# Kernel tuning notes

Measured on AMD Instinct MI355X. Metric: run time of the kernel, lower is better.

## Reference

```python
import jax, jax.numpy as jnp
import numpy as np

ALPHA = 0.2   # LeakyReLU negative slope
BN_EPS = 1e-5
NEG_INF = -9e15  # same masking constant as the torch source


def make_quaternion_mul(kernel):
    # kernel: [in_features//4, out_features]; returns hamilton [in_features, out_features]
    r, i, j, k = jnp.split(kernel, 4, axis=1)
    r2 = jnp.concatenate([r, -i, -j, -k], axis=1)
    i2 = jnp.concatenate([i,  r, -k,  j], axis=1)
    j2 = jnp.concatenate([j,  k,  r, -i], axis=1)
    k2 = jnp.concatenate([k, -j,  i,  r], axis=1)
    return jnp.concatenate([r2, i2, j2, k2], axis=0)


def setup_inputs() -> dict:
    key = jax.random.key(0)
    k1, k2, k3, k4 = jax.random.split(key, 4)
    N, IN_F, OUT_F = 8192, 1024, 256
    inp = jax.random.normal(k1, (N, IN_F), dtype=jnp.float32)
    adj = jax.random.randint(k2, (N, N), 0, 2, dtype=jnp.int32)
    # xavier-uniform-like init scales
    W = jax.random.uniform(k3, (IN_F // 4, OUT_F), dtype=jnp.float32,
                           minval=-1.0, maxval=1.0) * np.sqrt(6.0 / (IN_F // 4 + OUT_F))
    a = jax.random.uniform(k4, (2 * OUT_F, 1), dtype=jnp.float32,
                           minval=-1.0, maxval=1.0) * np.sqrt(6.0 / (2 * OUT_F + 1))
    gamma = jnp.ones((OUT_F,), dtype=jnp.float32)
    beta = jnp.zeros((OUT_F,), dtype=jnp.float32)
    return {"input": inp, "adj": adj, "W": W, "a": a, "gamma": gamma, "beta": beta}


def reference(input, adj, W, a, gamma, beta):
    hamilton = make_quaternion_mul(W)            # [IN_F, OUT_F]
    h = input @ hamilton                         # [N, OUT_F]
    F_out = h.shape[1]
    # e[i, j] = leakyrelu(concat(h_i, h_j) . a) = leakyrelu(h_i.a1 + h_j.a2)
    a1 = a[:F_out, 0]
    a2 = a[F_out:, 0]
    e = jax.nn.leaky_relu((h @ a1)[:, None] + (h @ a2)[None, :],
                          negative_slope=ALPHA)  # [N, N]
    e = jnp.where(adj > 0, e, NEG_INF)
    attention = jax.nn.softmax(e, axis=1)        # masked softmax over neighbors
    h_prime = attention @ h                      # [N, OUT_F]
    # BatchNorm1d (training mode: batch statistics, biased variance)
    mean = jnp.mean(h_prime, axis=0)
    var = jnp.var(h_prime, axis=0)
    h_norm = (h_prime - mean) * jax.lax.rsqrt(var + BN_EPS) * gamma + beta
    return jax.nn.elu(h_norm)                    # concat=True -> elu
```

## Files before the change

### kernel.cpp

```cpp
#include <hip/hip_runtime.h>
#include <stdint.h>

#define ALPHA 0.2f
#define LOG2E 1.4426950408889634f

typedef __attribute__((ext_vector_type(8))) short short8;
typedef __attribute__((ext_vector_type(4))) float f32x4;
typedef __attribute__((ext_vector_type(16))) float f32x16;
typedef __attribute__((ext_vector_type(4))) int int4v;
typedef __attribute__((ext_vector_type(2))) unsigned int uint2v;

#if __has_builtin(__builtin_amdgcn_exp2f)
#define EXP2(x) __builtin_amdgcn_exp2f(x)
#else
#define EXP2(x) exp2f(x)
#endif

__device__ __forceinline__ unsigned short f2bf(float x){
  union { float f; uint32_t u; } v; v.f = x;
  uint32_t u = v.u;
  u += 0x7FFFu + ((u >> 16) & 1u);
  return (unsigned short)(u >> 16);
}
__device__ __forceinline__ float bf2f(unsigned short s){
  union { uint32_t u; float f; } v; v.u = ((uint32_t)s) << 16; return v.f;
}
__device__ __forceinline__ unsigned encf(float x){
  unsigned u = __float_as_uint(x);
  return (u & 0x80000000u) ? ~u : (u | 0x80000000u);
}
__device__ __forceinline__ float decf(unsigned u){
  return (u & 0x80000000u) ? __uint_as_float(u & 0x7FFFFFFFu) : __uint_as_float(~u);
}

__global__ void k_ham(const float* __restrict__ W, unsigned short* __restrict__ hi,
                      unsigned short* __restrict__ lo, unsigned* __restrict__ S2enc,
                      float* __restrict__ gsum, float* __restrict__ gsumsq){
  if (blockIdx.x == 0){
    if (threadIdx.x == 0) S2enc[0] = 0u;
    gsum[threadIdx.x] = 0.f; gsumsq[threadIdx.x] = 0.f;
  }
  int id = blockIdx.x * 256 + threadIdx.x;
  int c = id >> 10, k = id & 1023;
  int b = k >> 8, r = k & 255;
  int cb = c >> 6, col = c & 63;
  const int   comp[4][4] = {{0,1,2,3},{1,0,3,2},{2,3,0,1},{3,2,1,0}};
  const float sgn [4][4] = {{1.f,-1.f,-1.f,-1.f},{1.f,1.f,-1.f,1.f},
                            {1.f,1.f,1.f,-1.f},{1.f,-1.f,1.f,1.f}};
  float v = sgn[b][cb] * W[r * 256 + comp[b][cb] * 64 + col];
  unsigned short h = f2bf(v);
  hi[id] = h;
  lo[id] = f2bf(v - bf2f(h));
}

__global__ __launch_bounds__(256) void k_gemm1(
    const float* __restrict__ inp, const unsigned short* __restrict__ hamHi,
    const unsigned short* __restrict__ hamLo, const float* __restrict__ avec,
    unsigned short* __restrict__ hT, float* __restrict__ s1s, float* __restrict__ s2s,
    unsigned* __restrict__ S2enc){
  int i0 = blockIdx.x * 32;
  int w = threadIdx.x >> 6, lane = threadIdx.x & 63;
  int mi = lane & 15, g = lane >> 4;
  int cbase = w * 64;
  f32x4 acc[2][4];
#pragma unroll
  for (int mf=0; mf<2; ++mf)
#pragma unroll
    for (int nf=0; nf<4; ++nf) acc[mf][nf] = (f32x4){0.f,0.f,0.f,0.f};

  for (int k0 = 0; k0 < 1024; k0 += 32){
    short8 ah[2], al[2];
#pragma unroll
    for (int mf=0; mf<2; ++mf){
      const float* ap = inp + (size_t)(i0 + 16*mf + mi) * 1024 + k0 + 8*g;
      f32x4 x0 = *(const f32x4*)ap;
      f32x4 x1 = *(const f32x4*)(ap + 4);
#pragma unroll
      for (int e=0; e<8; ++e){
        float x = (e < 4) ? x0[e] : x1[e-4];
        unsigned short h = f2bf(x);
        ah[mf][e] = (short)h;
        al[mf][e] = (short)f2bf(x - bf2f(h));
      }
    }
    short8 bh[4], bl[4];
#pragma unroll
    for (int nf=0; nf<4; ++nf){
      size_t off = (size_t)(cbase + 16*nf + mi) * 1024 + k0 + 8*g;
      bh[nf] = *(const short8*)(hamHi + off);
      bl[nf] = *(const short8*)(hamLo + off);
    }
#pragma unroll
    for (int mf=0; mf<2; ++mf)
#pragma unroll
      for (int nf=0; nf<4; ++nf){
        acc[mf][nf] = __builtin_amdgcn_mfma_f32_16x16x32_bf16(ah[mf], bh[nf], acc[mf][nf], 0,0,0);
        acc[mf][nf] = __builtin_amdgcn_mfma_f32_16x16x32_bf16(ah[mf], bl[nf], acc[mf][nf], 0,0,0);
        acc[mf][nf] = __builtin_amdgcn_mfma_f32_16x16x32_bf16(al[mf], bh[nf], acc[mf][nf], 0,0,0);
      }
  }
  float p1[2][4] = {{0,0,0,0},{0,0,0,0}}, p2[2][4] = {{0,0,0,0},{0,0,0,0}};
#pragma unroll
  for (int nf=0; nf<4; ++nf){
    int c = cbase + 16*nf + mi;
    float a1c = avec[c], a2c = avec[256 + c];
    int Sc = (c & 7) << 3;
#pragma unroll
    for (int mf=0; mf<2; ++mf){
      int ibase = i0 + 16*mf + 4*g;
      uint2v u;
      u[0] = (uint32_t)f2bf(acc[mf][nf][0]) | ((uint32_t)f2bf(acc[mf][nf][1]) << 16);
      u[1] = (uint32_t)f2bf(acc[mf][nf][2]) | ((uint32_t)f2bf(acc[mf][nf][3]) << 16);
      *(uint2v*)(hT + (size_t)c * 8192 + (size_t)(ibase ^ Sc)) = u;
#pragma unroll
      for (int rg=0; rg<4; ++rg){
        p1[mf][rg] += acc[mf][nf][rg] * a1c;
        p2[mf][rg] += acc[mf][nf][rg] * a2c;
      }
    }
  }
#pragma unroll
  for (int off=1; off<16; off<<=1){
#pragma unroll
    for (int mf=0; mf<2; ++mf)
#pragma unroll
      for (int rg=0; rg<4; ++rg){
        p1[mf][rg] += __shfl_xor(p1[mf][rg], off);
        p2[mf][rg] += __shfl_xor(p2[mf][rg], off);
      }
  }
  __shared__ float red1[4][32], red2[4][32];
  if (mi == 0){
#pragma unroll
    for (int mf=0; mf<2; ++mf)
#pragma unroll
      for (int rg=0; rg<4; ++rg){
        red1[w][16*mf + 4*g + rg] = p1[mf][rg];
        red2[w][16*mf + 4*g + rg] = p2[mf][rg];
      }
  }
  __syncthreads();
  if (threadIdx.x < 32){
    int r = threadIdx.x;
    float v1 = red1[0][r] + red1[1][r] + red1[2][r] + red1[3][r];
    float v2 = red2[0][r] + red2[1][r] + red2[2][r] + red2[3][r];
    s1s[i0 + r] = v1 * LOG2E;
    float v2s = v2 * LOG2E;
    s2s[i0 + r] = v2s;
    float m = v2s;
#pragma unroll
    for (int off=1; off<32; off<<=1) m = fmaxf(m, __shfl_xor(m, off));
    if (r == 0) atomicMax(S2enc, encf(m));
  }
}

#define STAGE(t, b) do { \
    _Pragma("unroll") \
    for (int r_ = 0; r_ < 8; ++r_){ \
      int ch_ = tid + r_*256; \
      const unsigned short* gp_ = hT + (size_t)(ch_ >> 3)*8192 + jw0 + (t)*64 + (ch_&7)*8; \
      __builtin_amdgcn_global_load_lds((const __attribute__((address_space(1))) void*)(const void*)gp_, \
          (__attribute__((address_space(3))) void*)(void*)&hbuf[(b)][ch_*8], 16, 0, 0); \
    } } while(0)

#define ALOAD(dst, t) do { \
    _Pragma("unroll") \
    for (int ks_ = 0; ks_ < 4; ++ks_){ \
      dst[2*ks_]   = *(const int4v*)(arow + (t)*64 + ks_*16); \
      dst[2*ks_+1] = *(const int4v*)(arow + (t)*64 + ks_*16 + 4); \
    } } while(0)

__global__ __launch_bounds__(256,1) void k_attn(
    const int* __restrict__ adj, const unsigned short* __restrict__ hT,
    const float* __restrict__ s1s, const float* __restrict__ s2s,
    const unsigned* __restrict__ S2enc, float* __restrict__ accp, float* __restrict__ Zp){
  __shared__ unsigned short hbuf[2][256*64];
  __shared__ float s2l[2048];
  const int tid = threadIdx.x;
  const int id = blockIdx.x;
  const int js = (id & 7) >> 1;
  const int rb = ((id >> 3) << 1) | (id & 1);
  const int w = tid >> 6, lane = tid & 63;
  const int r31 = lane & 31, hi = lane >> 5;
  const int i0w = rb * 128 + w * 32;
  const int jw0 = js * 2048;

  { f32x4 v0 = *(const f32x4*)(s2s + jw0 + tid*8);
    f32x4 v1 = *(const f32x4*)(s2s + jw0 + tid*8 + 4);
    *(f32x4*)&s2l[tid*8] = v0; *(f32x4*)&s2l[tid*8 + 4] = v1; }

  const float S2MAX = decf(S2enc[0]);
  const float s1v = s1s[i0w + r31];
  const float xm = s1v + S2MAX;
  const float m2 = fmaxf(xm, ALPHA * xm);
  const float P1 = s1v - m2;
  const float P2 = ALPHA * s1v - m2;

  const int* arow = adj + (size_t)(i0w + r31) * 8192 + jw0 + hi*8;

  f32x16 acc[8];
#pragma unroll
  for (int nf=0; nf<8; ++nf)
#pragma unroll
    for (int q=0; q<16; ++q) acc[nf][q] = 0.f;
  float zac = 0.f;

  int4v cur[8], nxt[8];
  ALOAD(cur, 0);
  STAGE(0, 0);
  __syncthreads();

  for (int tile = 0; tile < 32; ++tile){
    const int buf = tile & 1;
    if (tile < 31){
      STAGE(tile + 1, buf ^ 1);
      ALOAD(nxt, tile + 1);
    }
#pragma unroll
    for (int ks=0; ks<4; ++ks){
      f32x4 sa = *(const f32x4*)&s2l[tile*64 + ks*16 + hi*8];
      f32x4 sb = *(const f32x4*)&s2l[tile*64 + ks*16 + hi*8 + 4];
      short8 pa;
#pragma unroll
      for (int e=0; e<8; ++e){
        float s2e = (e < 4) ? sa[e] : sb[e-4];
        float t1 = P1 + s2e;
        float t2 = fmaf(ALPHA, s2e, P2);
        float pe = EXP2(fmaxf(t1, t2));
        int ae = (e < 4) ? cur[2*ks][e] : cur[2*ks+1][e-4];
        pe = (ae > 0) ? pe : 0.f;
        zac += pe;
        pa[e] = (short)f2bf(pe);
      }
      const int xk = ks*16 + hi*8;
#pragma unroll
      for (int nf=0; nf<8; ++nf){
        const int c = 32*nf + r31;
        short8 b = *(const short8*)&hbuf[buf][c*64 + (xk ^ ((c&7)<<3))];
        acc[nf] = __builtin_amdgcn_mfma_f32_32x32x16_bf16(pa, b, acc[nf], 0,0,0);
      }
    }
    if (tile < 31){
#pragma unroll
      for (int q=0; q<8; ++q) cur[q] = nxt[q];
    }
    __syncthreads();
  }
  zac += __shfl_xor(zac, 32);
  if (lane < 32) Zp[js*8192 + i0w + lane] = zac;
#pragma unroll
  for (int nf=0; nf<8; ++nf){
    const int c = 32*nf + r31;
#pragma unroll
    for (int reg=0; reg<16; ++reg){
      const int roff = (reg&3) + 8*(reg>>2) + 4*hi;
      accp[(size_t)(js*8192 + i0w + roff)*256 + c] = acc[nf][reg];
    }
  }
}

__global__ void k_stats(const float* __restrict__ accp, const float* __restrict__ Zp,
                        float* __restrict__ hp, float* __restrict__ gsum,
                        float* __restrict__ gsumsq){
  int c = threadIdx.x;
  int r0 = blockIdx.x * 32;
  float s = 0.f, sq = 0.f;
  for (int r=0; r<32; ++r){
    int i = r0 + r;
    float z = Zp[i] + Zp[8192 + i] + Zp[16384 + i] + Zp[24576 + i];
    float inv = (z > 0.f) ? 1.f / z : 0.f;
    size_t o = (size_t)i * 256 + c;
    float v = (accp[o] + accp[o + 8192*256] + accp[o + 2*8192*256] + accp[o + 3*8192*256]) * inv;
    hp[o] = v;
    s += v; sq += v*v;
  }
  atomicAdd(&gsum[c], s);
  atomicAdd(&gsumsq[c], sq);
}

__global__ void k_bnelu(float* __restrict__ out, const float* __restrict__ gsum,
                        const float* __restrict__ gsumsq, const float* __restrict__ gamma,
                        const float* __restrict__ beta){
  int id = blockIdx.x * 256 + threadIdx.x;
  int c = id & 255;
  float mean = gsum[c] * (1.f/8192.f);
  float var  = gsumsq[c] * (1.f/8192.f) - mean*mean;
  float x = (out[id] - mean) * rsqrtf(var + 1e-5f) * gamma[c] + beta[c];
  out[id] = x > 0.f ? x : (EXP2(x * LOG2E) - 1.f);
}

extern "C" void kernel_launch(void* const* d_in, const int* in_sizes, int n_in,
                              void* d_out, int out_size, void* d_ws, size_t ws_size,
                              hipStream_t stream){
  const float* inp   = (const float*)d_in[0];
  const int*   adj   = (const int*)d_in[1];
  const float* W     = (const float*)d_in[2];
  const float* avec  = (const float*)d_in[3];
  const float* gamma = (const float*)d_in[4];
  const float* beta  = (const float*)d_in[5];
  float* out = (float*)d_out;

  char* ws = (char*)d_ws;
  float* accp = (float*)ws;
  float* Zp   = accp + 4*8192*256;
  unsigned short* hamHi = (unsigned short*)(Zp + 32768);
  unsigned short* hamLo = hamHi + 262144;
  unsigned short* hT    = hamLo + 262144;
  float* s1s = (float*)(hT + 2097152);
  float* s2s = s1s + 8192;
  unsigned* S2enc = (unsigned*)(s2s + 8192);
  float* gsum   = (float*)(S2enc + 64);
  float* gsumsq = gsum + 256;

  k_ham<<<1024, 256, 0, stream>>>(W, hamHi, hamLo, S2enc, gsum, gsumsq);
  k_gemm1<<<256, 256, 0, stream>>>(inp, hamHi, hamLo, avec, hT, s1s, s2s, S2enc);
  k_attn<<<256, 256, 0, stream>>>(adj, hT, s1s, s2s, S2enc, accp, Zp);
  k_stats<<<256, 256, 0, stream>>>(accp, Zp, out, gsum, gsumsq);
  k_bnelu<<<8192, 256, 0, stream>>>(out, gsum, gsumsq, gamma, beta);
}
```

Baseline: 192.9 us.

## Pre-pack adjacency into bitmasks in a high-occupancy pass before attention

Extra blocks are added to the first GEMM launch that convert the int32 adjacency matrix into 64-bit ballot bitmasks. The attention kernel then reads one bit per edge instead of a full int, which removes the large adj stream from the low-occupancy MFMA loop. The full adjacency read still happens once, but at high occupancy, and it costs an extra bitmask buffer plus a kernel-ordering dependency.

```diff
diff --git a/kernel.cpp b/kernel.cpp
--- a/kernel.cpp
+++ b/kernel.cpp
@@ -53,11 +53,31 @@
   lo[id] = f2bf(v - bf2f(h));
 }
 
-__global__ __launch_bounds__(256) void k_gemm1(
-    const float* __restrict__ inp, const unsigned short* __restrict__ hamHi,
-    const unsigned short* __restrict__ hamLo, const float* __restrict__ avec,
-    unsigned short* __restrict__ hT, float* __restrict__ s1s, float* __restrict__ s2s,
-    unsigned* __restrict__ S2enc){
+__global__ __launch_bounds__(256) void k_work(
+    const float* __restrict__ inp, const int* __restrict__ adj,
+    const unsigned short* __restrict__ hamHi, const unsigned short* __restrict__ hamLo,
+    const float* __restrict__ avec, unsigned short* __restrict__ hT,
+    float* __restrict__ s1s, float* __restrict__ s2s, unsigned* __restrict__ S2enc,
+    unsigned long long* __restrict__ bm){
+  if (blockIdx.x >= 256){
+    const int lane = threadIdx.x & 63;
+    const size_t wid = ((size_t)(blockIdx.x - 256) * 256 + threadIdx.x) >> 6;
+    const size_t W0 = wid * 1024;
+    unsigned long long b[16];
+#pragma unroll
+    for (int q = 0; q < 4; ++q){
+      int4v a = *(const int4v*)(adj + W0 + 256*q + 4*lane);
+#pragma unroll
+      for (int k = 0; k < 4; ++k) b[4*q + k] = __ballot(a[k] > 0);
+    }
+    if (lane < 16){
+      unsigned long long v = b[0];
+#pragma unroll
+      for (int m = 1; m < 16; ++m) v = (lane == m) ? b[m] : v;
+      bm[W0/64 + lane] = v;
+    }
+    return;
+  }
   int i0 = blockIdx.x * 32;
   int w = threadIdx.x >> 6, lane = threadIdx.x & 63;
   int mi = lane & 15, g = lane >> 4;
@@ -163,15 +183,8 @@
           (__attribute__((address_space(3))) void*)(void*)&hbuf[(b)][ch_*8], 16, 0, 0); \
     } } while(0)
 
-#define ALOAD(dst, t) do { \
-    _Pragma("unroll") \
-    for (int ks_ = 0; ks_ < 4; ++ks_){ \
-      dst[2*ks_]   = *(const int4v*)(arow + (t)*64 + ks_*16); \
-      dst[2*ks_+1] = *(const int4v*)(arow + (t)*64 + ks_*16 + 4); \
-    } } while(0)
-
 __global__ __launch_bounds__(256,1) void k_attn(
-    const int* __restrict__ adj, const unsigned short* __restrict__ hT,
+    const unsigned long long* __restrict__ bm, const unsigned short* __restrict__ hT,
     const float* __restrict__ s1s, const float* __restrict__ s2s,
     const unsigned* __restrict__ S2enc, float* __restrict__ accp, float* __restrict__ Zp){
   __shared__ unsigned short hbuf[2][256*64];
@@ -196,7 +209,7 @@
   const float P1 = s1v - m2;
   const float P2 = ALPHA * s1v - m2;
 
-  const int* arow = adj + (size_t)(i0w + r31) * 8192 + jw0 + hi*8;
+  const unsigned long long* brow = bm + (size_t)(i0w + r31) * 128 + js * 32;
 
   f32x16 acc[8];
 #pragma unroll
@@ -205,21 +218,34 @@
     for (int q=0; q<16; ++q) acc[nf][q] = 0.f;
   float zac = 0.f;
 
-  int4v cur[8], nxt[8];
-  ALOAD(cur, 0);
+  unsigned long long Wc[4], Wn[4];
+#pragma unroll
+  for (int k=0;k<4;++k) Wc[k] = brow[k];
   STAGE(0, 0);
   __syncthreads();
 
   for (int tile = 0; tile < 32; ++tile){
     const int buf = tile & 1;
-    if (tile < 31){
-      STAGE(tile + 1, buf ^ 1);
-      ALOAD(nxt, tile + 1);
-    }
+    if ((tile & 3) == 0){
+      if (tile){
+#pragma unroll
+        for (int k=0;k<4;++k) Wc[k] = Wn[k];
+      }
+      if (tile + 4 < 32){
+        const unsigned long long* p = brow + (tile >> 2)*4 + 4;
+#pragma unroll
+        for (int k=0;k<4;++k) Wn[k] = p[k];
+      }
+    }
+    if (tile < 31) STAGE(tile + 1, buf ^ 1);
 #pragma unroll
     for (int ks=0; ks<4; ++ks){
       f32x4 sa = *(const f32x4*)&s2l[tile*64 + ks*16 + hi*8];
       f32x4 sb = *(const f32x4*)&s2l[tile*64 + ks*16 + hi*8 + 4];
+      const int sh0 = ((tile & 3) << 4) + (ks << 2) + (hi << 1);
+      unsigned tt[4];
+#pragma unroll
+      for (int k=0;k<4;++k) tt[k] = (unsigned)(Wc[k] >> sh0);
       short8 pa;
 #pragma unroll
       for (int e=0; e<8; ++e){
@@ -227,8 +253,7 @@
         float t1 = P1 + s2e;
         float t2 = fmaf(ALPHA, s2e, P2);
         float pe = EXP2(fmaxf(t1, t2));
-        int ae = (e < 4) ? cur[2*ks][e] : cur[2*ks+1][e-4];
-        pe = (ae > 0) ? pe : 0.f;
+        pe = ((tt[e & 3] >> (e >> 2)) & 1u) ? pe : 0.f;
         zac += pe;
         pa[e] = (short)f2bf(pe);
       }
@@ -239,10 +264,6 @@
         short8 b = *(const short8*)&hbuf[buf][c*64 + (xk ^ ((c&7)<<3))];
         acc[nf] = __builtin_amdgcn_mfma_f32_32x32x16_bf16(pa, b, acc[nf], 0,0,0);
       }
-    }
-    if (tile < 31){
-#pragma unroll
-      for (int q=0; q<8; ++q) cur[q] = nxt[q];
     }
     __syncthreads();
   }
@@ -311,10 +332,11 @@
   unsigned* S2enc = (unsigned*)(s2s + 8192);
   float* gsum   = (float*)(S2enc + 64);
   float* gsumsq = gsum + 256;
+  unsigned long long* bm = (unsigned long long*)(gsumsq + 256);
 
   k_ham<<<1024, 256, 0, stream>>>(W, hamHi, hamLo, S2enc, gsum, gsumsq);
-  k_gemm1<<<256, 256, 0, stream>>>(inp, hamHi, hamLo, avec, hT, s1s, s2s, S2enc);
-  k_attn<<<256, 256, 0, stream>>>(adj, hT, s1s, s2s, S2enc, accp, Zp);
+  k_work<<<16640, 256, 0, stream>>>(inp, adj, hamHi, hamLo, avec, hT, s1s, s2s, S2enc, bm);
+  k_attn<<<256, 256, 0, stream>>>(bm, hT, s1s, s2s, S2enc, accp, Zp);
   k_stats<<<256, 256, 0, stream>>>(accp, Zp, out, gsum, gsumsq);
   k_bnelu<<<8192, 256, 0, stream>>>(out, gsum, gsumsq, gamma, beta);
 }
```

After: 177.3 us. 1.09x faster.
